# Kernel tuning notes

Hardware: AMD Instinct MI355X
Metric: run time of the kernel (lower is better)

## Reference

```python
import jax, jax.numpy as jnp
import numpy as np

B_J0 = 0.01
BETA = 1.8
GAMMA = 0.5
LENS = 0.5
HIGHT = 0.15
SCALE = 6.0
H1, H2, D_IN, D_OUT = 256, 256, 700, 20
BATCH, T = 128, 250


def spike_fn(x):
    # forward of ActFun_adp: Heaviside
    return (x > 0).astype(x.dtype)


def mem_update_adp(inputs, mem, spike, tau_adp, b, tau_m):
    alpha = jnp.exp(-1.0 / tau_m)
    ro = jnp.exp(-1.0 / tau_adp)
    b = ro * b + (1.0 - ro) * spike
    B = B_J0 + BETA * b
    mem = mem * alpha + (1.0 - alpha) * inputs - B * spike
    spike = spike_fn(mem - B)
    return mem, spike, b


def setup_inputs() -> dict:
    key = jax.random.key(0)
    ks = jax.random.split(key, 16)
    inp = {
        "x": jax.random.uniform(ks[0], (BATCH, T, D_IN), jnp.float32),
        "mem1_0": jax.random.uniform(ks[1], (BATCH, H1), jnp.float32),
        "mem2_0": jax.random.uniform(ks[2], (BATCH, H2), jnp.float32),
        "memo_0": jax.random.uniform(ks[3], (BATCH, D_OUT), jnp.float32),
        "Wi1": jax.random.normal(ks[4], (H1, D_IN), jnp.float32) * 0.05,
        "bi1": jnp.zeros((H1,), jnp.float32),
        "W11": jax.random.normal(ks[5], (H1, H1), jnp.float32) * 0.05,
        "b11": jnp.zeros((H1,), jnp.float32),
        "W12": jax.random.normal(ks[6], (H2, H1), jnp.float32) * 0.05,
        "b12": jnp.zeros((H2,), jnp.float32),
        "W22": jax.random.normal(ks[7], (H2, H2), jnp.float32) * 0.05,
        "b22": jnp.zeros((H2,), jnp.float32),
        "Wo": jax.random.normal(ks[8], (D_OUT, H2), jnp.float32) * 0.05,
        "bo": jnp.zeros((D_OUT,), jnp.float32),
        "tau_adp_h1": 150.0 + 10.0 * jax.random.normal(ks[9], (H1,), jnp.float32),
        "tau_adp_h2": 150.0 + 10.0 * jax.random.normal(ks[10], (H2,), jnp.float32),
        "tau_m_h1": 20.0 + 5.0 * jax.random.normal(ks[11], (H1,), jnp.float32),
        "tau_m_h2": 20.0 + 5.0 * jax.random.normal(ks[12], (H2,), jnp.float32),
        "tau_m_o": 20.0 + 5.0 * jax.random.normal(ks[13], (D_OUT,), jnp.float32),
    }
    return inp


def reference(x, mem1_0, mem2_0, memo_0, Wi1, bi1, W11, b11, W12, b12,
              W22, b22, Wo, bo, tau_adp_h1, tau_adp_h2, tau_m_h1, tau_m_h2, tau_m_o):
    B = x.shape[0]
    sp1_0 = jnp.zeros_like(mem1_0)
    sp2_0 = jnp.zeros_like(mem2_0)
    b1_0 = jnp.full_like(mem1_0, B_J0)
    b2_0 = jnp.full_like(mem2_0, B_J0)
    acc0 = jnp.zeros((B, Wo.shape[0]), x.dtype)
    alpha_o = jnp.exp(-1.0 / tau_m_o)

    def step(carry, inp):
        x_t, i = inp
        mem1, sp1, b1, mem2, sp2, b2, memo, acc = carry
        h1_in = x_t @ Wi1.T + bi1 + sp1 @ W11.T + b11
        mem1, sp1, b1 = mem_update_adp(h1_in, mem1, sp1, tau_adp_h1, b1, tau_m_h1)
        h2_in = sp1 @ W12.T + b12 + sp2 @ W22.T + b22
        mem2, sp2, b2 = mem_update_adp(h2_in, mem2, sp2, tau_adp_h2, b2, tau_m_h2)
        memo = memo * alpha_o + (1.0 - alpha_o) * (sp2 @ Wo.T + bo)
        acc = acc + jnp.where(i > 10, jax.nn.softmax(memo, axis=1), 0.0)
        return (mem1, sp1, b1, mem2, sp2, b2, memo, acc), None

    xs = jnp.swapaxes(x, 0, 1)  # [T, B, D_in]
    ts = jnp.arange(xs.shape[0])
    carry, _ = jax.lax.scan(step, (mem1_0, sp1_0, b1_0, mem2_0, sp2_0, b2_0, memo_0, acc0), (xs, ts))
    return carry[-1]  # accumulated softmax output [B, D_out]
```

## Files before the change

kernel.cpp:

```cpp
#include <hip/hip_runtime.h>
#include <math.h>

#define BATCH 128
#define T 250
#define D_IN 700
#define H 256
#define D_OUT 20

typedef float v2f __attribute__((ext_vector_type(2)));
typedef __attribute__((ext_vector_type(8))) short bf16x8;
typedef __attribute__((ext_vector_type(4))) float f32x4;

static __device__ __forceinline__ unsigned short f2b(float f) {
    unsigned u = __float_as_uint(f);
    u += 0x7FFFu + ((u >> 16) & 1u);
    return (unsigned short)(u >> 16);
}

static __device__ __forceinline__ void bar() {
    asm volatile("s_waitcnt lgkmcnt(0)" ::: "memory");
    __builtin_amdgcn_s_barrier();
    asm volatile("" ::: "memory");
}

#define PIDX(c) (10 * ((c) >> 3) + ((c) & 7))

#define N_C  (257 * 512)
#define N_WP (256 * 704)

__global__ void prep_k(const float* __restrict__ Wi1, const float* __restrict__ W11,
                       const float* __restrict__ W12, const float* __restrict__ W22,
                       const float* __restrict__ Wo,
                       unsigned short* __restrict__ Wi1p, float* __restrict__ C1f,
                       float* __restrict__ C2f) {
    int idx = blockIdx.x * 256 + threadIdx.x;
    if (idx < N_C) {
        int k = idx >> 9, p = idx & 511;
        float v = 0.f;
        if (k < H) v = (p < 256) ? W12[p * H + k] : W11[(p - 256) * H + k];
        C1f[idx] = v;
        return;
    }
    idx -= N_C;
    if (idx < N_C) {
        int k = idx >> 9, p = idx & 511;
        float v = 0.f;
        if (k < H) {
            if (p < 256) v = W22[p * H + k];
            else if (p - 256 < D_OUT) v = Wo[(p - 256) * H + k];
        }
        C2f[idx] = v;
        return;
    }
    idx -= N_C;
    if (idx < N_WP) {
        int h = idx / 704, k = idx - h * 704;
        Wi1p[idx] = (k < D_IN) ? f2b(Wi1[h * D_IN + k]) : (unsigned short)0;
    }
}

__global__ __launch_bounds__(256) void gemm_u_k(const float* __restrict__ x,
                                                const unsigned short* __restrict__ Wi1p,
                                                const float* __restrict__ bi1,
                                                float* __restrict__ U) {
    const int lane = threadIdx.x & 63;
    const int wv = threadIdx.x >> 6;
    const int quad = lane >> 4;
    const int nl = lane & 15;
    const int mbase = blockIdx.x * 64 + wv * 16;
    const int m = mbase + nl;

    f32x4 acc[16];
#pragma unroll
    for (int i = 0; i < 16; ++i) acc[i] = (f32x4)(0.f);

    float bias[16];
#pragma unroll
    for (int nt = 0; nt < 16; ++nt) bias[nt] = bi1[nt * 16 + nl];

    const float* xrow = x + (size_t)m * D_IN;
    const unsigned short* brow = Wi1p + nl * 704 + quad * 8;

    for (int k0 = 0; k0 < 704; k0 += 32) {
        int ka = k0 + quad * 8;
        int ka2 = (ka + 4 <= 696) ? ka + 4 : 696;
        float4 q0 = *(const float4*)(xrow + ka);
        float4 q1 = *(const float4*)(xrow + ka2);
        bf16x8 af;
        af[0] = (short)f2b(q0.x); af[1] = (short)f2b(q0.y);
        af[2] = (short)f2b(q0.z); af[3] = (short)f2b(q0.w);
        af[4] = (short)f2b(q1.x); af[5] = (short)f2b(q1.y);
        af[6] = (short)f2b(q1.z); af[7] = (short)f2b(q1.w);

        const unsigned short* bp = brow + k0;
        bf16x8 bf[16];
#pragma unroll
        for (int nt = 0; nt < 16; ++nt)
            bf[nt] = *(const bf16x8*)(bp + nt * 16 * 704);
#pragma unroll
        for (int nt = 0; nt < 16; ++nt)
            acc[nt] = __builtin_amdgcn_mfma_f32_16x16x32_bf16(af, bf[nt], acc[nt], 0, 0, 0);
    }

#pragma unroll
    for (int nt = 0; nt < 16; ++nt) {
#pragma unroll
        for (int r = 0; r < 4; ++r) {
            U[(size_t)(mbase + quad * 4 + r) * H + nt * 16 + nl] = acc[nt][r] + bias[nt];
        }
    }
}

static __device__ __forceinline__ void ld8f(const unsigned* __restrict__ L, int c,
                                            const float* __restrict__ Cb, unsigned l8,
                                            f32x4* ba, f32x4* bb) {
    uint4 ia = *(const uint4*)(L + c);
    uint4 ib = *(const uint4*)(L + c + 4);
    unsigned I[8] = {ia.x, ia.y, ia.z, ia.w, ib.x, ib.y, ib.z, ib.w};
#pragma unroll
    for (int j = 0; j < 8; ++j) {
        const float* p = Cb + ((unsigned)I[j] << 9) + l8;
        ba[j] = *(const f32x4*)p;
        bb[j] = *(const f32x4*)(p + 4);
    }
}

static __device__ __forceinline__ void acc8(const f32x4* ba, const f32x4* bb,
                                            f32x4& A0, f32x4& A1) {
#pragma unroll
    for (int j = 0; j < 8; ++j) { A0 += ba[j]; A1 += bb[j]; }
}

static __device__ __forceinline__ void gather8(const unsigned* __restrict__ L, int n,
                                               const float* __restrict__ Cb, unsigned l8,
                                               f32x4& A0, f32x4& A1) {
    A0 = (f32x4)(0.f);
    A1 = (f32x4)(0.f);
    int nr = (n + 7) & ~7;
    if (nr == 0) return;
    f32x4 xa[8], xb[8], ya[8], yb[8];
    ld8f(L, 0, Cb, l8, xa, xb);
    if (nr == 8) { acc8(xa, xb, A0, A1); return; }
    ld8f(L, 8, Cb, l8, ya, yb);
    int c = 16;
    for (; c + 16 <= nr; c += 16) {
        acc8(xa, xb, A0, A1); ld8f(L, c, Cb, l8, xa, xb);
        acc8(ya, yb, A0, A1); ld8f(L, c + 8, Cb, l8, ya, yb);
    }
    if (nr - c == 8) {
        acc8(xa, xb, A0, A1); ld8f(L, c, Cb, l8, xa, xb);
        acc8(ya, yb, A0, A1); acc8(xa, xb, A0, A1);
    } else {
        acc8(xa, xb, A0, A1); acc8(ya, yb, A0, A1);
    }
}

__global__ __launch_bounds__(256, 1) void recurrent_k(
    const float* __restrict__ U,
    const float* __restrict__ mem1_0, const float* __restrict__ mem2_0,
    const float* __restrict__ memo_0,
    const float* __restrict__ b11v, const float* __restrict__ b12v,
    const float* __restrict__ b22v, const float* __restrict__ bov,
    const float* __restrict__ tau_adp_h1, const float* __restrict__ tau_adp_h2,
    const float* __restrict__ tau_m_h1, const float* __restrict__ tau_m_h2,
    const float* __restrict__ tau_m_o,
    const float* __restrict__ C1f, const float* __restrict__ C2f,
    float* __restrict__ out)
{
    const int tid = threadIdx.x;
    const int lane = tid & 63;
    const int w = tid >> 6;
    const int hw = w & 1;
    const bool trackA = (w < 2);
    const int bi = blockIdx.x;
    const int th = hw * 64 + lane;
    const int n0 = 2 * th;
    const unsigned woff = hw * 128;
    const unsigned l8 = (unsigned)lane * 8;

    __shared__ float PA[2][2][640];
    __shared__ float PB[2][3][640];
    __shared__ __align__(16) unsigned lists[4][192];

    for (int i = tid; i < 2 * 2 * 640; i += 256) ((float*)PA)[i] = 0.f;
    for (int i = tid; i < 2 * 3 * 640; i += 256) ((float*)PB)[i] = 0.f;
    __syncthreads();

    v2f mem1 = (v2f)(0.f), b1v = (v2f)(0.f), spk1 = (v2f)(0.f);
    v2f al1 = (v2f)(0.f), ro1 = (v2f)(0.f), oma1 = (v2f)(0.f), omr1 = (v2f)(0.f);
    v2f b11p = (v2f)(0.f);
    if (trackA) {
        mem1 = *(const v2f*)(mem1_0 + bi * H + n0);
        b1v = (v2f)(0.01f);
        v2f tm = *(const v2f*)(tau_m_h1 + n0);
        v2f ta = *(const v2f*)(tau_adp_h1 + n0);
        al1.x = __expf(-1.f / tm.x); al1.y = __expf(-1.f / tm.y);
        ro1.x = __expf(-1.f / ta.x); ro1.y = __expf(-1.f / ta.y);
        oma1 = 1.f - al1; omr1 = 1.f - ro1;
        b11p = *(const v2f*)(b11v + n0);
    }

    v2f mem2 = (v2f)(0.f), b2v = (v2f)(0.f), spk2 = (v2f)(0.f);
    v2f al2 = (v2f)(0.f), ro2 = (v2f)(0.f), oma2 = (v2f)(0.f), omr2 = (v2f)(0.f);
    v2f bs2 = (v2f)(0.f);
    if (!trackA) {
        mem2 = *(const v2f*)(mem2_0 + bi * H + n0);
        b2v = (v2f)(0.01f);
        v2f tm = *(const v2f*)(tau_m_h2 + n0);
        v2f ta = *(const v2f*)(tau_adp_h2 + n0);
        al2.x = __expf(-1.f / tm.x); al2.y = __expf(-1.f / tm.y);
        ro2.x = __expf(-1.f / ta.x); ro2.y = __expf(-1.f / ta.y);
        oma2 = 1.f - al2; omr2 = 1.f - ro2;
        bs2 = *(const v2f*)(b12v + n0) + *(const v2f*)(b22v + n0);
    }

    v2f memo = (v2f)(0.f), alo = (v2f)(0.f), omo = (v2f)(0.f);
    v2f bop = (v2f)(0.f), acco = (v2f)(0.f);
    const bool outlane = (w == 2 && lane < 10);
    if (outlane) {
        memo = *(const v2f*)(memo_0 + bi * D_OUT + 2 * lane);
        v2f tm = *(const v2f*)(tau_m_o + 2 * lane);
        alo.x = __expf(-1.f / tm.x); alo.y = __expf(-1.f / tm.y);
        omo = 1.f - alo;
        bop = *(const v2f*)(bov + 2 * lane);
    }

    const float* Up = U + (size_t)bi * T * H + n0;
    v2f u_cur = (v2f)(0.f), u_nxt = (v2f)(0.f);
    if (trackA) u_cur = *(const v2f*)Up;
    const unsigned long long below = (1ull << lane) - 1ull;

    for (int t = 0; t < 252; ++t) {
        const int rbA = (t + 1) & 1;
        const int wbA = t & 1;
        const int rsB = (t + 1) % 3;
        const int wsB = (t + 2) % 3;

        if (trackA && t < 250) {
            v2f g11 = *(const v2f*)&PA[0][rbA][PIDX(256 + n0)] +
                      *(const v2f*)&PA[1][rbA][PIDX(256 + n0)];
            v2f h1 = u_cur + b11p + g11;
            b1v = ro1 * b1v + omr1 * spk1;
            v2f B1 = 0.01f + 1.8f * b1v;
            mem1 = mem1 * al1 + oma1 * h1 - B1 * spk1;
            v2f d = mem1 - B1;
            spk1.x = (d.x > 0.f) ? 1.f : 0.f;
            spk1.y = (d.y > 0.f) ? 1.f : 0.f;

            unsigned long long m0 = __ballot(spk1.x != 0.f);
            unsigned long long m1 = __ballot(spk1.y != 0.f);
            int c0 = __popcll(m0);
            int n = c0 + __popcll(m1);
            unsigned* L = lists[w];
            if (spk1.x != 0.f) L[__popcll(m0 & below)] = woff + 2 * lane;
            if (spk1.y != 0.f) L[c0 + __popcll(m1 & below)] = woff + 2 * lane + 1;
            L[n + lane] = 256u;
            asm volatile("s_waitcnt lgkmcnt(0)" ::: "memory");
            __builtin_amdgcn_wave_barrier();

            if (t + 1 < 250) u_nxt = *(const v2f*)(Up + H);
            Up += H;

            f32x4 A0, A1;
            gather8(L, n, C1f, l8, A0, A1);

            float* pw = &PA[hw][wbA][10 * lane];
            const v2f* ap = (const v2f*)&A0;
            const v2f* bp = (const v2f*)&A1;
            *(v2f*)(pw + 0) = ap[0];
            *(v2f*)(pw + 2) = ap[1];
            *(v2f*)(pw + 4) = bp[0];
            *(v2f*)(pw + 6) = bp[1];

            u_cur = u_nxt;
        }

        if (w == 2 && t >= 2) {
            v2f e = (v2f)(0.f);
            if (lane < 10) {
                v2f aO = *(const v2f*)&PB[0][rsB][PIDX(256 + 2 * lane)] +
                         *(const v2f*)&PB[1][rsB][PIDX(256 + 2 * lane)];
                memo = memo * alo + omo * (bop + aO);
                e.x = __expf(memo.x);
                e.y = __expf(memo.y);
            }
            if (t >= 13) {
                float s = e.x + e.y;
#pragma unroll
                for (int dd = 8; dd >= 1; dd >>= 1) s += __shfl_xor(s, dd, 16);
                if (lane < 10) acco += e * __fdividef(1.f, s);
            }
        }

        if (!trackA && t >= 1 && t < 251) {
            v2f g12 = *(const v2f*)&PA[0][rbA][PIDX(n0)] +
                      *(const v2f*)&PA[1][rbA][PIDX(n0)];
            v2f g22 = *(const v2f*)&PB[0][rsB][PIDX(n0)] +
                      *(const v2f*)&PB[1][rsB][PIDX(n0)];
            v2f h2 = bs2 + g22 + g12;
            b2v = ro2 * b2v + omr2 * spk2;
            v2f B2 = 0.01f + 1.8f * b2v;
            mem2 = mem2 * al2 + oma2 * h2 - B2 * spk2;
            v2f d = mem2 - B2;
            spk2.x = (d.x > 0.f) ? 1.f : 0.f;
            spk2.y = (d.y > 0.f) ? 1.f : 0.f;

            unsigned long long m0 = __ballot(spk2.x != 0.f);
            unsigned long long m1 = __ballot(spk2.y != 0.f);
            int c0 = __popcll(m0);
            int n = c0 + __popcll(m1);
            unsigned* L = lists[w];
            if (spk2.x != 0.f) L[__popcll(m0 & below)] = woff + 2 * lane;
            if (spk2.y != 0.f) L[c0 + __popcll(m1 & below)] = woff + 2 * lane + 1;
            L[n + lane] = 256u;
            asm volatile("s_waitcnt lgkmcnt(0)" ::: "memory");
            __builtin_amdgcn_wave_barrier();

            f32x4 A0, A1;
            gather8(L, n, C2f, l8, A0, A1);

            float* pw = &PB[hw][wsB][10 * lane];
            const v2f* ap = (const v2f*)&A0;
            const v2f* bp = (const v2f*)&A1;
            *(v2f*)(pw + 0) = ap[0];
            *(v2f*)(pw + 2) = ap[1];
            *(v2f*)(pw + 4) = bp[0];
            *(v2f*)(pw + 6) = bp[1];
        }

        bar();
    }

    if (outlane) {
        *(v2f*)(out + bi * D_OUT + 2 * lane) = acco;
    }
}

extern "C" void kernel_launch(void* const* d_in, const int* in_sizes, int n_in,
                              void* d_out, int out_size, void* d_ws, size_t ws_size,
                              hipStream_t stream) {
    const float* x          = (const float*)d_in[0];
    const float* mem1_0     = (const float*)d_in[1];
    const float* mem2_0     = (const float*)d_in[2];
    const float* memo_0     = (const float*)d_in[3];
    const float* Wi1        = (const float*)d_in[4];
    const float* bi1        = (const float*)d_in[5];
    const float* W11        = (const float*)d_in[6];
    const float* b11        = (const float*)d_in[7];
    const float* W12        = (const float*)d_in[8];
    const float* b12        = (const float*)d_in[9];
    const float* W22        = (const float*)d_in[10];
    const float* b22        = (const float*)d_in[11];
    const float* Wo         = (const float*)d_in[12];
    const float* bo         = (const float*)d_in[13];
    const float* tau_adp_h1 = (const float*)d_in[14];
    const float* tau_adp_h2 = (const float*)d_in[15];
    const float* tau_m_h1   = (const float*)d_in[16];
    const float* tau_m_h2   = (const float*)d_in[17];
    const float* tau_m_o    = (const float*)d_in[18];

    float* U = (float*)d_ws;
    float* C1f = U + ((size_t)BATCH * T + 1) * H;
    float* C2f = C1f + N_C;
    unsigned short* Wi1p = (unsigned short*)(C2f + N_C);

    int prep_total = 2 * N_C + N_WP;
    prep_k<<<(prep_total + 255) / 256, 256, 0, stream>>>(
        Wi1, W11, W12, W22, Wo, Wi1p, C1f, C2f);

    gemm_u_k<<<(BATCH * T) / 64, 256, 0, stream>>>(x, Wi1p, bi1, U);

    recurrent_k<<<BATCH, 256, 0, stream>>>(U, mem1_0, mem2_0, memo_0,
                                           b11, b12, b22, bo,
                                           tau_adp_h1, tau_adp_h2,
                                           tau_m_h1, tau_m_h2, tau_m_o,
                                           C1f, C2f, (float*)d_out);
}
```

Measured before the change: 439.1 us.

## Store recurrent weight tables in bf16 and split neurons across eight waves

The recurrent weight tables used by the spike-driven gather are stored as bf16 instead of fp32, halving the bytes loaded per spiking neuron. The recurrent block grows from 256 to 512 threads so that each lane owns one neuron instead of two. Each wave's spike list is therefore shorter, which shortens the serial gather chain per step, at the cost of four partial sums to reduce through shared memory instead of two. The bf16 weights reduce accuracy in the spike threshold comparisons, which could flip spikes.

```diff
diff --git a/kernel.cpp b/kernel.cpp
--- a/kernel.cpp
+++ b/kernel.cpp
@@ -10,6 +10,7 @@
 typedef float v2f __attribute__((ext_vector_type(2)));
 typedef __attribute__((ext_vector_type(8))) short bf16x8;
 typedef __attribute__((ext_vector_type(4))) float f32x4;
+typedef __attribute__((ext_vector_type(4))) unsigned u32x4;
 
 static __device__ __forceinline__ unsigned short f2b(float f) {
     unsigned u = __float_as_uint(f);
@@ -31,14 +32,14 @@
 __global__ void prep_k(const float* __restrict__ Wi1, const float* __restrict__ W11,
                        const float* __restrict__ W12, const float* __restrict__ W22,
                        const float* __restrict__ Wo,
-                       unsigned short* __restrict__ Wi1p, float* __restrict__ C1f,
-                       float* __restrict__ C2f) {
+                       unsigned short* __restrict__ Wi1p, unsigned short* __restrict__ C1,
+                       unsigned short* __restrict__ C2) {
     int idx = blockIdx.x * 256 + threadIdx.x;
     if (idx < N_C) {
         int k = idx >> 9, p = idx & 511;
         float v = 0.f;
         if (k < H) v = (p < 256) ? W12[p * H + k] : W11[(p - 256) * H + k];
-        C1f[idx] = v;
+        C1[idx] = f2b(v);
         return;
     }
     idx -= N_C;
@@ -49,7 +50,7 @@
             if (p < 256) v = W22[p * H + k];
             else if (p - 256 < D_OUT) v = Wo[(p - 256) * H + k];
         }
-        C2f[idx] = v;
+        C2[idx] = f2b(v);
         return;
     }
     idx -= N_C;
@@ -111,51 +112,55 @@
     }
 }
 
-static __device__ __forceinline__ void ld8f(const unsigned* __restrict__ L, int c,
-                                            const float* __restrict__ Cb, unsigned l8,
-                                            f32x4* ba, f32x4* bb) {
+static __device__ __forceinline__ void ld8b(const unsigned* __restrict__ L, int c,
+                                            const unsigned short* __restrict__ Cb,
+                                            unsigned l8, u32x4* b) {
     uint4 ia = *(const uint4*)(L + c);
     uint4 ib = *(const uint4*)(L + c + 4);
     unsigned I[8] = {ia.x, ia.y, ia.z, ia.w, ib.x, ib.y, ib.z, ib.w};
 #pragma unroll
-    for (int j = 0; j < 8; ++j) {
-        const float* p = Cb + ((unsigned)I[j] << 9) + l8;
-        ba[j] = *(const f32x4*)p;
-        bb[j] = *(const f32x4*)(p + 4);
-    }
-}
-
-static __device__ __forceinline__ void acc8(const f32x4* ba, const f32x4* bb,
-                                            f32x4& A0, f32x4& A1) {
-#pragma unroll
-    for (int j = 0; j < 8; ++j) { A0 += ba[j]; A1 += bb[j]; }
-}
-
-static __device__ __forceinline__ void gather8(const unsigned* __restrict__ L, int n,
-                                               const float* __restrict__ Cb, unsigned l8,
-                                               f32x4& A0, f32x4& A1) {
-    A0 = (f32x4)(0.f);
-    A1 = (f32x4)(0.f);
+    for (int jj = 0; jj < 8; ++jj)
+        b[jj] = *(const u32x4*)(Cb + ((unsigned)I[jj] << 9) + l8);
+}
+
+static __device__ __forceinline__ void acc8b(const u32x4* b, v2f* a) {
+#pragma unroll
+    for (int jj = 0; jj < 8; ++jj) {
+#pragma unroll
+        for (int q = 0; q < 4; ++q) {
+            unsigned u = b[jj][q];
+            v2f t;
+            t.x = __uint_as_float(u << 16);
+            t.y = __uint_as_float(u & 0xffff0000u);
+            a[q] += t;
+        }
+    }
+}
+
+static __device__ __forceinline__ void gatherB(const unsigned* __restrict__ L, int n,
+                                               const unsigned short* __restrict__ Cb,
+                                               unsigned l8, v2f* a) {
+    a[0] = (v2f)(0.f); a[1] = (v2f)(0.f); a[2] = (v2f)(0.f); a[3] = (v2f)(0.f);
     int nr = (n + 7) & ~7;
     if (nr == 0) return;
-    f32x4 xa[8], xb[8], ya[8], yb[8];
-    ld8f(L, 0, Cb, l8, xa, xb);
-    if (nr == 8) { acc8(xa, xb, A0, A1); return; }
-    ld8f(L, 8, Cb, l8, ya, yb);
+    u32x4 x[8], y[8];
+    ld8b(L, 0, Cb, l8, x);
+    if (nr == 8) { acc8b(x, a); return; }
+    ld8b(L, 8, Cb, l8, y);
     int c = 16;
     for (; c + 16 <= nr; c += 16) {
-        acc8(xa, xb, A0, A1); ld8f(L, c, Cb, l8, xa, xb);
-        acc8(ya, yb, A0, A1); ld8f(L, c + 8, Cb, l8, ya, yb);
+        acc8b(x, a); ld8b(L, c, Cb, l8, x);
+        acc8b(y, a); ld8b(L, c + 8, Cb, l8, y);
     }
     if (nr - c == 8) {
-        acc8(xa, xb, A0, A1); ld8f(L, c, Cb, l8, xa, xb);
-        acc8(ya, yb, A0, A1); acc8(xa, xb, A0, A1);
+        acc8b(x, a); ld8b(L, c, Cb, l8, x);
+        acc8b(y, a); acc8b(x, a);
     } else {
-        acc8(xa, xb, A0, A1); acc8(ya, yb, A0, A1);
-    }
-}
-
-__global__ __launch_bounds__(256, 1) void recurrent_k(
+        acc8b(x, a); acc8b(y, a);
+    }
+}
+
+__global__ __launch_bounds__(512, 1) void recurrent_k(
     const float* __restrict__ U,
     const float* __restrict__ mem1_0, const float* __restrict__ mem2_0,
     const float* __restrict__ memo_0,
@@ -164,71 +169,63 @@
     const float* __restrict__ tau_adp_h1, const float* __restrict__ tau_adp_h2,
     const float* __restrict__ tau_m_h1, const float* __restrict__ tau_m_h2,
     const float* __restrict__ tau_m_o,
-    const float* __restrict__ C1f, const float* __restrict__ C2f,
+    const unsigned short* __restrict__ C1b, const unsigned short* __restrict__ C2b,
     float* __restrict__ out)
 {
     const int tid = threadIdx.x;
     const int lane = tid & 63;
     const int w = tid >> 6;
-    const int hw = w & 1;
-    const bool trackA = (w < 2);
+    const bool trackA = (w < 4);
+    const int wt = w & 3;
     const int bi = blockIdx.x;
-    const int th = hw * 64 + lane;
-    const int n0 = 2 * th;
-    const unsigned woff = hw * 128;
+    const int j = wt * 64 + lane;
     const unsigned l8 = (unsigned)lane * 8;
 
-    __shared__ float PA[2][2][640];
-    __shared__ float PB[2][3][640];
-    __shared__ __align__(16) unsigned lists[4][192];
-
-    for (int i = tid; i < 2 * 2 * 640; i += 256) ((float*)PA)[i] = 0.f;
-    for (int i = tid; i < 2 * 3 * 640; i += 256) ((float*)PB)[i] = 0.f;
+    __shared__ float PA[4][2][640];
+    __shared__ float PB[4][3][640];
+    __shared__ __align__(16) unsigned lists[8][128];
+
+    for (int i = tid; i < 4 * 2 * 640; i += 512) ((float*)PA)[i] = 0.f;
+    for (int i = tid; i < 4 * 3 * 640; i += 512) ((float*)PB)[i] = 0.f;
     __syncthreads();
 
-    v2f mem1 = (v2f)(0.f), b1v = (v2f)(0.f), spk1 = (v2f)(0.f);
-    v2f al1 = (v2f)(0.f), ro1 = (v2f)(0.f), oma1 = (v2f)(0.f), omr1 = (v2f)(0.f);
-    v2f b11p = (v2f)(0.f);
+    float mem1 = 0.f, b1 = 0.01f, spk1 = 0.f;
+    float al1 = 0.f, ro1 = 0.f, oma1 = 0.f, omr1 = 0.f, b11p = 0.f;
     if (trackA) {
-        mem1 = *(const v2f*)(mem1_0 + bi * H + n0);
-        b1v = (v2f)(0.01f);
-        v2f tm = *(const v2f*)(tau_m_h1 + n0);
-        v2f ta = *(const v2f*)(tau_adp_h1 + n0);
-        al1.x = __expf(-1.f / tm.x); al1.y = __expf(-1.f / tm.y);
-        ro1.x = __expf(-1.f / ta.x); ro1.y = __expf(-1.f / ta.y);
+        mem1 = mem1_0[bi * H + j];
+        al1 = __expf(-1.f / tau_m_h1[j]);
+        ro1 = __expf(-1.f / tau_adp_h1[j]);
         oma1 = 1.f - al1; omr1 = 1.f - ro1;
-        b11p = *(const v2f*)(b11v + n0);
-    }
-
-    v2f mem2 = (v2f)(0.f), b2v = (v2f)(0.f), spk2 = (v2f)(0.f);
-    v2f al2 = (v2f)(0.f), ro2 = (v2f)(0.f), oma2 = (v2f)(0.f), omr2 = (v2f)(0.f);
-    v2f bs2 = (v2f)(0.f);
+        b11p = b11v[j];
+    }
+
+    float mem2 = 0.f, b2 = 0.01f, spk2 = 0.f;
+    float al2 = 0.f, ro2 = 0.f, oma2 = 0.f, omr2 = 0.f, bs2 = 0.f;
     if (!trackA) {
-        mem2 = *(const v2f*)(mem2_0 + bi * H + n0);
-        b2v = (v2f)(0.01f);
-        v2f tm = *(const v2f*)(tau_m_h2 + n0);
-        v2f ta = *(const v2f*)(tau_adp_h2 + n0);
-        al2.x = __expf(-1.f / tm.x); al2.y = __expf(-1.f / tm.y);
-        ro2.x = __expf(-1.f / ta.x); ro2.y = __expf(-1.f / ta.y);
+        mem2 = mem2_0[bi * H + j];
+        al2 = __expf(-1.f / tau_m_h2[j]);
+        ro2 = __expf(-1.f / tau_adp_h2[j]);
         oma2 = 1.f - al2; omr2 = 1.f - ro2;
-        bs2 = *(const v2f*)(b12v + n0) + *(const v2f*)(b22v + n0);
-    }
-
-    v2f memo = (v2f)(0.f), alo = (v2f)(0.f), omo = (v2f)(0.f);
-    v2f bop = (v2f)(0.f), acco = (v2f)(0.f);
-    const bool outlane = (w == 2 && lane < 10);
-    if (outlane) {
-        memo = *(const v2f*)(memo_0 + bi * D_OUT + 2 * lane);
-        v2f tm = *(const v2f*)(tau_m_o + 2 * lane);
-        alo.x = __expf(-1.f / tm.x); alo.y = __expf(-1.f / tm.y);
+        bs2 = b12v[j] + b22v[j];
+    }
+
+    float memo = 0.f, alo = 0.f, omo = 0.f, bop = 0.f, acco = 0.f;
+    const bool outl = (w == 4 && lane < D_OUT);
+    if (outl) {
+        memo = memo_0[bi * D_OUT + lane];
+        alo = __expf(-1.f / tau_m_o[lane]);
         omo = 1.f - alo;
-        bop = *(const v2f*)(bov + 2 * lane);
-    }
-
-    const float* Up = U + (size_t)bi * T * H + n0;
-    v2f u_cur = (v2f)(0.f), u_nxt = (v2f)(0.f);
-    if (trackA) u_cur = *(const v2f*)Up;
+        bop = bov[lane];
+    }
+
+    const float* Up = U + (size_t)bi * T * H + j;
+    float u_cur = trackA ? *Up : 0.f;
+    float u_nxt = 0.f;
     const unsigned long long below = (1ull << lane) - 1ull;
+
+    const int pidx_self = 320 + PIDX(j);
+    const int pidx_j = PIDX(j);
+    const int pidx_out = 320 + PIDX(lane);
 
     for (int t = 0; t < 252; ++t) {
         const int rbA = (t + 1) & 1;
@@ -237,103 +234,85 @@
         const int wsB = (t + 2) % 3;
 
         if (trackA && t < 250) {
-            v2f g11 = *(const v2f*)&PA[0][rbA][PIDX(256 + n0)] +
-                      *(const v2f*)&PA[1][rbA][PIDX(256 + n0)];
-            v2f h1 = u_cur + b11p + g11;
-            b1v = ro1 * b1v + omr1 * spk1;
-            v2f B1 = 0.01f + 1.8f * b1v;
+            float g11 = PA[0][rbA][pidx_self] + PA[1][rbA][pidx_self] +
+                        PA[2][rbA][pidx_self] + PA[3][rbA][pidx_self];
+            float h1 = u_cur + b11p + g11;
+            b1 = ro1 * b1 + omr1 * spk1;
+            float B1 = 0.01f + 1.8f * b1;
             mem1 = mem1 * al1 + oma1 * h1 - B1 * spk1;
-            v2f d = mem1 - B1;
-            spk1.x = (d.x > 0.f) ? 1.f : 0.f;
-            spk1.y = (d.y > 0.f) ? 1.f : 0.f;
-
-            unsigned long long m0 = __ballot(spk1.x != 0.f);
-            unsigned long long m1 = __ballot(spk1.y != 0.f);
-            int c0 = __popcll(m0);
-            int n = c0 + __popcll(m1);
+            spk1 = (mem1 - B1 > 0.f) ? 1.f : 0.f;
+
+            unsigned long long m = __ballot(spk1 != 0.f);
+            int n = __popcll(m);
             unsigned* L = lists[w];
-            if (spk1.x != 0.f) L[__popcll(m0 & below)] = woff + 2 * lane;
-            if (spk1.y != 0.f) L[c0 + __popcll(m1 & below)] = woff + 2 * lane + 1;
+            if (spk1 != 0.f) L[__popcll(m & below)] = (unsigned)j;
             L[n + lane] = 256u;
             asm volatile("s_waitcnt lgkmcnt(0)" ::: "memory");
             __builtin_amdgcn_wave_barrier();
 
-            if (t + 1 < 250) u_nxt = *(const v2f*)(Up + H);
+            u_nxt = Up[H];
             Up += H;
 
-            f32x4 A0, A1;
-            gather8(L, n, C1f, l8, A0, A1);
-
-            float* pw = &PA[hw][wbA][10 * lane];
-            const v2f* ap = (const v2f*)&A0;
-            const v2f* bp = (const v2f*)&A1;
-            *(v2f*)(pw + 0) = ap[0];
-            *(v2f*)(pw + 2) = ap[1];
-            *(v2f*)(pw + 4) = bp[0];
-            *(v2f*)(pw + 6) = bp[1];
-
+            v2f a[4];
+            gatherB(L, n, C1b, l8, a);
+
+            float* pw = &PA[wt][wbA][10 * lane];
+            *(v2f*)(pw + 0) = a[0];
+            *(v2f*)(pw + 2) = a[1];
+            *(v2f*)(pw + 4) = a[2];
+            *(v2f*)(pw + 6) = a[3];
             u_cur = u_nxt;
         }
 
-        if (w == 2 && t >= 2) {
-            v2f e = (v2f)(0.f);
-            if (lane < 10) {
-                v2f aO = *(const v2f*)&PB[0][rsB][PIDX(256 + 2 * lane)] +
-                         *(const v2f*)&PB[1][rsB][PIDX(256 + 2 * lane)];
+        if (w == 4 && t >= 2) {
+            float e = 0.f;
+            if (lane < D_OUT) {
+                float aO = PB[0][rsB][pidx_out] + PB[1][rsB][pidx_out] +
+                           PB[2][rsB][pidx_out] + PB[3][rsB][pidx_out];
                 memo = memo * alo + omo * (bop + aO);
-                e.x = __expf(memo.x);
-                e.y = __expf(memo.y);
+                e = __expf(memo);
             }
             if (t >= 13) {
-                float s = e.x + e.y;
-#pragma unroll
-                for (int dd = 8; dd >= 1; dd >>= 1) s += __shfl_xor(s, dd, 16);
-                if (lane < 10) acco += e * __fdividef(1.f, s);
+                float s = e;
+#pragma unroll
+                for (int dd = 16; dd >= 1; dd >>= 1) s += __shfl_xor(s, dd, 32);
+                if (lane < D_OUT) acco += __fdividef(e, s);
             }
         }
 
         if (!trackA && t >= 1 && t < 251) {
-            v2f g12 = *(const v2f*)&PA[0][rbA][PIDX(n0)] +
-                      *(const v2f*)&PA[1][rbA][PIDX(n0)];
-            v2f g22 = *(const v2f*)&PB[0][rsB][PIDX(n0)] +
-                      *(const v2f*)&PB[1][rsB][PIDX(n0)];
-            v2f h2 = bs2 + g22 + g12;
-            b2v = ro2 * b2v + omr2 * spk2;
-            v2f B2 = 0.01f + 1.8f * b2v;
+            float g12 = PA[0][rbA][pidx_j] + PA[1][rbA][pidx_j] +
+                        PA[2][rbA][pidx_j] + PA[3][rbA][pidx_j];
+            float g22 = PB[0][rsB][pidx_j] + PB[1][rsB][pidx_j] +
+                        PB[2][rsB][pidx_j] + PB[3][rsB][pidx_j];
+            float h2 = bs2 + g22 + g12;
+            b2 = ro2 * b2 + omr2 * spk2;
+            float B2 = 0.01f + 1.8f * b2;
             mem2 = mem2 * al2 + oma2 * h2 - B2 * spk2;
-            v2f d = mem2 - B2;
-            spk2.x = (d.x > 0.f) ? 1.f : 0.f;
-            spk2.y = (d.y > 0.f) ? 1.f : 0.f;
-
-            unsigned long long m0 = __ballot(spk2.x != 0.f);
-            unsigned long long m1 = __ballot(spk2.y != 0.f);
-            int c0 = __popcll(m0);
-            int n = c0 + __popcll(m1);
+            spk2 = (mem2 - B2 > 0.f) ? 1.f : 0.f;
+
+            unsigned long long m = __ballot(spk2 != 0.f);
+            int n = __popcll(m);
             unsigned* L = lists[w];
-            if (spk2.x != 0.f) L[__popcll(m0 & below)] = woff + 2 * lane;
-            if (spk2.y != 0.f) L[c0 + __popcll(m1 & below)] = woff + 2 * lane + 1;
+            if (spk2 != 0.f) L[__popcll(m & below)] = (unsigned)j;
             L[n + lane] = 256u;
             asm volatile("s_waitcnt lgkmcnt(0)" ::: "memory");
             __builtin_amdgcn_wave_barrier();
 
-            f32x4 A0, A1;
-            gather8(L, n, C2f, l8, A0, A1);
-
-            float* pw = &PB[hw][wsB][10 * lane];
-            const v2f* ap = (const v2f*)&A0;
-            const v2f* bp = (const v2f*)&A1;
-            *(v2f*)(pw + 0) = ap[0];
-            *(v2f*)(pw + 2) = ap[1];
-            *(v2f*)(pw + 4) = bp[0];
-            *(v2f*)(pw + 6) = bp[1];
+            v2f a[4];
+            gatherB(L, n, C2b, l8, a);
+
+            float* pw = &PB[wt][wsB][10 * lane];
+            *(v2f*)(pw + 0) = a[0];
+            *(v2f*)(pw + 2) = a[1];
+            *(v2f*)(pw + 4) = a[2];
+            *(v2f*)(pw + 6) = a[3];
         }
 
         bar();
     }
 
-    if (outlane) {
-        *(v2f*)(out + bi * D_OUT + 2 * lane) = acco;
-    }
+    if (outl) out[bi * D_OUT + lane] = acco;
 }
 
 extern "C" void kernel_launch(void* const* d_in, const int* in_sizes, int n_in,
@@ -360,19 +339,19 @@
     const float* tau_m_o    = (const float*)d_in[18];
 
     float* U = (float*)d_ws;
-    float* C1f = U + ((size_t)BATCH * T + 1) * H;
-    float* C2f = C1f + N_C;
-    unsigned short* Wi1p = (unsigned short*)(C2f + N_C);
+    unsigned short* C1b = (unsigned short*)(U + ((size_t)BATCH * T + 1) * H);
+    unsigned short* C2b = C1b + N_C;
+    unsigned short* Wi1p = C2b + N_C;
 
     int prep_total = 2 * N_C + N_WP;
     prep_k<<<(prep_total + 255) / 256, 256, 0, stream>>>(
-        Wi1, W11, W12, W22, Wo, Wi1p, C1f, C2f);
+        Wi1, W11, W12, W22, Wo, Wi1p, C1b, C2b);
 
     gemm_u_k<<<(BATCH * T) / 64, 256, 0, stream>>>(x, Wi1p, bi1, U);
 
-    recurrent_k<<<BATCH, 256, 0, stream>>>(U, mem1_0, mem2_0, memo_0,
+    recurrent_k<<<BATCH, 512, 0, stream>>>(U, mem1_0, mem2_0, memo_0,
                                            b11, b12, b22, bo,
                                            tau_adp_h1, tau_adp_h2,
                                            tau_m_h1, tau_m_h2, tau_m_o,
-                                           C1f, C2f, (float*)d_out);
-}
+                                           C1b, C2b, (float*)d_out);
+}
```

Result: faster. 384.9 us, median of 2 (-12.4%).
